# Optimization experiments

Measured on AMD Instinct MI355X. Metric: run time of the kernel, lower is better.

The kernel has to match this reference:

```python
import jax, jax.numpy as jnp
import numpy as np

N = 768          # n_nuclei
EMB = 32         # embedding_dim
RBF = 32         # rbf_dim
CUTOFF = 10.0    # rbf_cutoff
MAXQ = 10        # max(charges)


def _edges(n):
    # fully-connected edge list exactly as in GNN.__call__
    senders = np.arange(n).repeat(n - 1)
    recv = np.arange(n)[None].repeat(n - 1, axis=0)
    recv = (recv + np.arange(n - 1)[:, None] + 1) % n
    return jnp.asarray(senders), jnp.asarray(recv.reshape(-1))


def _mlp2(x, w0, b0, w1, b1=None):
    # AutoMLP(out_dim, depth=2): Dense+silu, Dense (final_bias optional)
    h = jax.nn.silu(x @ w0 + b0)
    y = h @ w1
    return y if b1 is None else y + b1


def _seg_mean(vals, seg, n):
    s = jax.ops.segment_sum(vals, seg, num_segments=n, indices_are_sorted=True)
    c = jax.ops.segment_sum(jnp.ones((vals.shape[0], 1), vals.dtype), seg,
                            num_segments=n, indices_are_sorted=True)
    return s / jnp.maximum(c, 1.0)


def setup_inputs() -> dict:
    key = jax.random.key(0)
    ki = iter(jax.random.split(key, 48))

    def W(din, dout):
        return jax.random.normal(next(ki), (din, dout), jnp.float32) / np.sqrt(din).astype(np.float32)

    def b(d):
        return jax.random.normal(next(ki), (d,), jnp.float32) * 0.01

    return dict(
        nuclei=jax.random.normal(next(ki), (N, 3), jnp.float32) * 3.0,
        charges=jax.random.randint(next(ki), (N,), 0, MAXQ),
        f=(jnp.arange(RBF, dtype=jnp.float32) + 1.0) * jnp.pi,  # BesselRBF param init
        embed_table=jax.random.normal(next(ki), (MAXQ, EMB), jnp.float32),
        mp1_w0=W(96, 32), mp1_b0=b(32), mp1_w1=W(32, 32), mp1_b1=b(32),
        up1_w0=W(64, 64), up1_b0=b(64), up1_w1=W(64, 64), up1_b1=b(64),
        mp2_w0=W(160, 32), mp2_b0=b(32), mp2_w1=W(32, 32), mp2_b1=b(32),
        up2_w0=W(96, 64), up2_b0=b(64), up2_w1=W(64, 64), up2_b1=b(64),
        no_w0=W(160, 3), no_b0=b(3), no_w1=W(3, 3),
        no_embed=jax.random.normal(next(ki), (MAXQ, 3), jnp.float32) * 0.1,
        go_w0=W(160, 1), go_b0=b(1), go_w1=W(1, 1), go_b1=b(1),
    )


def reference(nuclei, charges, f, embed_table,
              mp1_w0, mp1_b0, mp1_w1, mp1_b1,
              up1_w0, up1_b0, up1_w1, up1_b1,
              mp2_w0, mp2_b0, mp2_w1, mp2_b1,
              up2_w0, up2_b0, up2_w1, up2_b1,
              no_w0, no_b0, no_w1, no_embed,
              go_w0, go_b0, go_w1, go_b1):
    nuclei = nuclei.reshape(-1, 3) @ jnp.eye(3, dtype=nuclei.dtype)  # constants 'axes'
    n = nuclei.shape[0]
    senders, receivers = _edges(n)

    # BesselRBF on pairwise distances
    d = jnp.linalg.norm(nuclei[senders] - nuclei[receivers], axis=-1)
    x_ext = d[:, None] + 1e-8
    e_embed = jnp.sqrt(2.0 / CUTOFF) * jnp.sin(f * x_ext / CUTOFF) / x_ext  # [E, RBF]

    n_embed = embed_table[charges]  # [N, EMB]
    embeddings = [n_embed]

    # layer 1: msg out 32, update out 64 (no residual: 32 != 64)
    edge_in = jnp.concatenate([n_embed[senders], n_embed[receivers], e_embed], axis=-1)
    msg = _seg_mean(_mlp2(edge_in, mp1_w0, mp1_b0, mp1_w1, mp1_b1), senders, n)
    upd = _mlp2(jnp.concatenate([n_embed, msg], axis=-1), up1_w0, up1_b0, up1_w1, up1_b1)
    n_embed = upd  # dims differ -> plain replacement
    embeddings.append(n_embed)

    # layer 2: msg out 32, update out 64 (residual: 64 == 64)
    edge_in = jnp.concatenate([n_embed[senders], n_embed[receivers], e_embed], axis=-1)
    msg = _seg_mean(_mlp2(edge_in, mp2_w0, mp2_b0, mp2_w1, mp2_b1), senders, n)
    upd = _mlp2(jnp.concatenate([n_embed, msg], axis=-1), up2_w0, up2_b0, up2_w1, up2_b1)
    n_embed = n_embed + upd
    embeddings.append(n_embed)

    agg = jnp.concatenate(embeddings, axis=-1)  # [N, 32+64+64=160]

    node_out = _mlp2(agg, no_w0, no_b0, no_w1) + no_embed[charges]  # [N, 3]
    global_out = _mlp2(jnp.mean(agg, axis=0), go_w0, go_b0, go_w1, go_b1)  # [1]
    return (node_out, global_out)
```

## Files before the change

### kernel.cpp

```cpp
#include <hip/hip_runtime.h>
#include <hip/hip_bf16.h>

typedef __hip_bfloat16 bf16;
typedef __attribute__((ext_vector_type(8))) short short8;
typedef __attribute__((ext_vector_type(4))) float float4v;

#define NN   768
#define NEPS 767

#define C_NUC   0
#define C_F     2304
#define C_MP1W0 2656
#define C_MP1B0 5728
#define C_MP1W1 5760
#define C_MP1B1 6784
#define C_UP1W0 6816
#define C_UP1B0 10912
#define C_UP1W1 10976
#define C_UP1B1 15072
#define C_MP2W0 15136
#define C_MP2B0 20256
#define C_MP2W1 20288
#define C_MP2B1 21312
#define C_UP2W0 21344
#define C_UP2B0 27488
#define C_UP2W1 27552
#define C_UP2B1 31648
#define C_NOW0  31712
#define C_NOB0  32192
#define C_NOW1  32195
#define C_NOEMB 32204
#define C_GOW0  32234
#define C_GOB0  32394
#define C_GOW1  32395
#define C_GOB1  32396
#define C_ETAB  32400
__device__ __align__(16) float g_c[32720];

#define OFF_EMB1 73728
#define OFF_SA2  122880
#define OFF_SB2  147456
__device__ float g_ws[172032];
__device__ float g_agg[640];
__device__ float g_tab[660];
__device__ int   g_cnt;
__device__ int   g_isf;
__device__ short8 g_rbf[NN*48*64];

struct Ptrs { const void* p[28]; };

__device__ __forceinline__ float b2f(bf16 v){ return __bfloat162float(v); }
__device__ __forceinline__ float LD(const void* p, int i, int f32){
  return f32 ? ((const float*)p)[i] : b2f(((const bf16*)p)[i]);
}
__device__ __forceinline__ int detect_f32(const void* f){
  float v = ((const float*)f)[0];
  return (fabsf(v - 3.14159265f) < 0.01f) ? 1 : 0;
}
__device__ __forceinline__ float fast_rcp(float x){ return __builtin_amdgcn_rcpf(x); }
__device__ __forceinline__ float silu_f(float p){ return p * fast_rcp(1.f + __expf(-p)); }
__device__ __forceinline__ unsigned short rne_bf16(float x){
  unsigned int b = __float_as_uint(x);
  return (unsigned short)((b + 0x7fffu + ((b >> 16) & 1u)) >> 16);
}
__device__ __forceinline__ void cv(const void* p, int off, int sz, int gt, int isf){
  for (int i = gt; i < sz; i += 96*256) g_c[off + i] = LD(p, i, isf);
}

__launch_bounds__(256)
__global__ void k_conv_prep(Ptrs P){
  int t = threadIdx.x;
  int gt = blockIdx.x*256 + t;
  int isf = detect_f32(P.p[2]);
  if (gt == 0){ g_isf = isf; g_cnt = 0; }
  if (gt < 640) g_agg[gt] = 0.f;

  cv(P.p[0],  C_NUC,   2304, gt, isf);
  cv(P.p[2],  C_F,     32,   gt, isf);
  cv(P.p[3],  C_ETAB,  320,  gt, isf);
  cv(P.p[4],  C_MP1W0, 3072, gt, isf);
  cv(P.p[5],  C_MP1B0, 32,   gt, isf);
  cv(P.p[6],  C_MP1W1, 1024, gt, isf);
  cv(P.p[7],  C_MP1B1, 32,   gt, isf);
  cv(P.p[8],  C_UP1W0, 4096, gt, isf);
  cv(P.p[9],  C_UP1B0, 64,   gt, isf);
  cv(P.p[10], C_UP1W1, 4096, gt, isf);
  cv(P.p[11], C_UP1B1, 64,   gt, isf);
  cv(P.p[12], C_MP2W0, 5120, gt, isf);
  cv(P.p[13], C_MP2B0, 32,   gt, isf);
  cv(P.p[14], C_MP2W1, 1024, gt, isf);
  cv(P.p[15], C_MP2B1, 32,   gt, isf);
  cv(P.p[16], C_UP2W0, 6144, gt, isf);
  cv(P.p[17], C_UP2B0, 64,   gt, isf);
  cv(P.p[18], C_UP2W1, 4096, gt, isf);
  cv(P.p[19], C_UP2B1, 64,   gt, isf);
  cv(P.p[20], C_NOW0,  480,  gt, isf);
  cv(P.p[21], C_NOB0,  3,    gt, isf);
  cv(P.p[22], C_NOW1,  9,    gt, isf);
  cv(P.p[23], C_NOEMB, 30,   gt, isf);
  cv(P.p[24], C_GOW0,  160,  gt, isf);
  cv(P.p[25], C_GOB0,  1,    gt, isf);
  cv(P.p[26], C_GOW1,  1,    gt, isf);
  cv(P.p[27], C_GOB1,  1,    gt, isf);

  if (blockIdx.x == 0){
    __shared__ float etabL[320], w0L[2048];
    for (int idx = t; idx < 320;  idx += 256) etabL[idx] = LD(P.p[3], idx, isf);
    for (int idx = t; idx < 2048; idx += 256) w0L[idx]   = LD(P.p[4], idx, isf);
    __syncthreads();
    for (int idx = t; idx < 320; idx += 256){
      int ch = idx >> 5, cc = idx & 31;
      float a = 0.f, b = 0.f;
      #pragma unroll
      for (int k = 0; k < 32; k++){
        float e = etabL[ch*32 + k];
        a = fmaf(e, w0L[k*32 + cc],        a);
        b = fmaf(e, w0L[1024 + k*32 + cc], b);
      }
      g_tab[ch*33 + cc]       = a;
      g_tab[330 + ch*33 + cc] = b;
    }
  }
}

__launch_bounds__(256)
__global__ void k_edge1(const int* __restrict__ charges){
  __shared__ __align__(16) float pos[NN*3];
  __shared__ __align__(16) float w1L[1024];
  __shared__ float TAL[330], TBL[330];
  __shared__ int   chS[NN];
  __shared__ float wsum[4][32];
  __shared__ float hsumL[32];
  __shared__ float msgL[32];
  __shared__ float catU[64], hU[64], e1U[64], part[256];

  int i = blockIdx.x, t = threadIdx.x;
  int w = t >> 6, lane = t & 63, q = lane >> 4, c = lane & 15;

  {
    const float4* src = (const float4*)(g_c + C_NUC);
    float4* dst = (float4*)pos;
    for (int idx = t; idx < 576; idx += 256) dst[idx] = src[idx];
    ((float4*)w1L)[t] = ((const float4*)(g_c + C_MP1W1))[t];
    for (int idx = t; idx < 660; idx += 256){
      float v = g_tab[idx];
      if (idx < 330) TAL[idx] = v; else TBL[idx - 330] = v;
    }
    for (int idx = t; idx < NN; idx += 256) chS[idx] = charges[idx];
  }
  short8 bfr0, bfr1;
  #pragma unroll
  for (int j = 0; j < 8; j++){
    int row = q*8 + j;
    bfr0[j] = (short)rne_bf16(g_c[C_MP1W0 + 2048 + row*32 + c]);
    bfr1[j] = (short)rne_bf16(g_c[C_MP1W0 + 2048 + row*32 + 16 + c]);
  }
  float fj[8];
  #pragma unroll
  for (int j = 0; j < 8; j++) fj[j] = g_c[C_F + q*8 + j] * 0.1f;
  __syncthreads();

  int chI = chS[i];
  float preB0 = TAL[chI*33 + c]      + g_c[C_MP1B0 + c];
  float preB1 = TAL[chI*33 + 16 + c] + g_c[C_MP1B0 + 16 + c];
  float px = pos[i*3], py = pos[i*3+1], pz = pos[i*3+2];

  float xs[12], scv[12];
  #pragma unroll
  for (int s = 0; s < 12; s++){
    int el = (w + s*4)*16 + c;
    int ela = (el < NEPS) ? el : 0;
    int r = ela + (ela >= i);
    float dx = px - pos[r*3], dy = py - pos[r*3+1], dz = pz - pos[r*3+2];
    float d = sqrtf(fmaf(dx, dx, fmaf(dy, dy, dz*dz)));
    xs[s] = d + 1e-8f;
    scv[s] = 0.44721359549995793f * fast_rcp(xs[s]);
  }

  float sum0 = 0.f, sum1 = 0.f;
  #pragma unroll 4
  for (int s = 0; s < 12; s++){
    int tl = w + s*4;
    float sb0[4], sb1[4];
    #pragma unroll
    for (int p = 0; p < 4; p++){
      int el2 = tl*16 + q*4 + p;
      int e2a = (el2 < NEPS) ? el2 : 0;
      int r2 = e2a + (e2a >= i);
      int ch2 = chS[r2];
      sb0[p] = TBL[ch2*33 + c];
      sb1[p] = TBL[ch2*33 + 16 + c];
    }
    short8 af;
    #pragma unroll
    for (int j = 0; j < 8; j++) af[j] = (short)rne_bf16(scv[s] * __sinf(fj[j]*xs[s]));
    g_rbf[(i*48 + tl)*64 + lane] = af;
    float4v z = {0.f, 0.f, 0.f, 0.f};
    float4v a0 = __builtin_amdgcn_mfma_f32_16x16x32_bf16(af, bfr0, z, 0, 0, 0);
    float4v a1 = __builtin_amdgcn_mfma_f32_16x16x32_bf16(af, bfr1, z, 0, 0, 0);
    #pragma unroll
    for (int p = 0; p < 4; p++){
      int el2 = tl*16 + q*4 + p;
      if (el2 < NEPS){
        sum0 += silu_f(a0[p] + preB0 + sb0[p]);
        sum1 += silu_f(a1[p] + preB1 + sb1[p]);
      }
    }
  }
  sum0 += __shfl_xor(sum0, 16); sum0 += __shfl_xor(sum0, 32);
  sum1 += __shfl_xor(sum1, 16); sum1 += __shfl_xor(sum1, 32);
  if (lane < 16){ wsum[w][lane] = sum0; wsum[w][16 + lane] = sum1; }
  __syncthreads();
  if (t < 32) hsumL[t] = wsum[0][t] + wsum[1][t] + wsum[2][t] + wsum[3][t];
  __syncthreads();
  if (t < 32){
    float y = 0.f;
    #pragma unroll
    for (int m = 0; m < 32; m++) y = fmaf(hsumL[m], w1L[m*32 + t], y);
    msgL[t] = y * (1.f/767.f) + g_c[C_MP1B1 + t];
  }

  if (t < 32){
    catU[t] = g_c[C_ETAB + chI*32 + t];
    catU[32 + t] = msgL[t];
  }
  __syncthreads();

  int g = t >> 6, col = t & 63;
  {
    const float* w0 = g_c + C_UP1W0;
    float p0 = 0.f;
    #pragma unroll
    for (int j = 0; j < 16; j++){ int k = g*16 + j; p0 = fmaf(catU[k], w0[k*64 + col], p0); }
    part[t] = p0;
  }
  __syncthreads();
  if (t < 64) hU[t] = silu_f(g_c[C_UP1B0 + t] + part[t] + part[64+t] + part[128+t] + part[192+t]);
  __syncthreads();
  {
    const float* w1u = g_c + C_UP1W1;
    float p1 = 0.f;
    #pragma unroll
    for (int j = 0; j < 16; j++){ int k = g*16 + j; p1 = fmaf(hU[k], w1u[k*64 + col], p1); }
    part[t] = p1;
  }
  __syncthreads();
  if (t < 64){
    float y = g_c[C_UP1B1 + t] + part[t] + part[64+t] + part[128+t] + part[192+t];
    e1U[t] = y;
    g_ws[OFF_EMB1 + i*64 + t] = y;
  }
  __syncthreads();
  {
    int half = t >> 7, g2 = (t >> 5) & 3, c32 = t & 31;
    const float* m2 = g_c + C_MP2W0;
    float p2 = 0.f;
    #pragma unroll
    for (int j = 0; j < 16; j++){
      int k = g2*16 + j;
      p2 = fmaf(e1U[k], m2[(half*64 + k)*32 + c32], p2);
    }
    part[t] = p2;
  }
  __syncthreads();
  if (t < 64){
    int half = t >> 5, c32 = t & 31;
    float s = part[half*128 + c32] + part[half*128 + 32 + c32]
            + part[half*128 + 64 + c32] + part[half*128 + 96 + c32];
    if (half == 0) g_ws[OFF_SA2 + i*32 + c32] = s;
    else           g_ws[OFF_SB2 + i*32 + c32] = s;
  }
}

__launch_bounds__(256)
__global__ void k_edge2(const int* __restrict__ charges, void* __restrict__ out){
  __shared__ __align__(16) float w1L[1024];
  __shared__ float wsum[4][32];
  __shared__ float hsumL[32];
  __shared__ float msgL[32];
  __shared__ float catU[96], hU[64], aggL[160], noL[522], h3L[3], part[256];
  __shared__ int lastL;

  int i = blockIdx.x, t = threadIdx.x;
  int w = t >> 6, lane = t & 63, q = lane >> 4, c = lane & 15;

  ((float4*)w1L)[t] = ((const float4*)(g_c + C_MP2W1))[t];
  const float* SA = g_ws + OFF_SA2;
  const float* SB = g_ws + OFF_SB2;
  short8 bfr0, bfr1;
  #pragma unroll
  for (int j = 0; j < 8; j++){
    int row = q*8 + j;
    bfr0[j] = (short)rne_bf16(g_c[C_MP2W0 + 4096 + row*32 + c]);
    bfr1[j] = (short)rne_bf16(g_c[C_MP2W0 + 4096 + row*32 + 16 + c]);
  }
  float preB0 = SA[i*32 + c]      + g_c[C_MP2B0 + c];
  float preB1 = SA[i*32 + 16 + c] + g_c[C_MP2B0 + 16 + c];

  float sum0 = 0.f, sum1 = 0.f;
  short8 afA = g_rbf[(i*48 + w)*64 + lane];
  float sbA0[4], sbA1[4];
  #pragma unroll
  for (int p = 0; p < 4; p++){
    int el2 = w*16 + q*4 + p;
    int e2a = (el2 < NEPS) ? el2 : 0;
    int r2 = e2a + (e2a >= i);
    sbA0[p] = SB[r2*32 + c];
    sbA1[p] = SB[r2*32 + 16 + c];
  }
  #pragma unroll
  for (int s = 0; s < 12; s++){
    int tl = w + s*4;
    short8 afB;
    float sbB0[4], sbB1[4];
    if (s < 11){
      int tn = tl + 4;
      afB = g_rbf[(i*48 + tn)*64 + lane];
      #pragma unroll
      for (int p = 0; p < 4; p++){
        int el2 = tn*16 + q*4 + p;
        int e2a = (el2 < NEPS) ? el2 : 0;
        int r2 = e2a + (e2a >= i);
        sbB0[p] = SB[r2*32 + c];
        sbB1[p] = SB[r2*32 + 16 + c];
      }
    }
    float4v z = {0.f, 0.f, 0.f, 0.f};
    float4v a0 = __builtin_amdgcn_mfma_f32_16x16x32_bf16(afA, bfr0, z, 0, 0, 0);
    float4v a1 = __builtin_amdgcn_mfma_f32_16x16x32_bf16(afA, bfr1, z, 0, 0, 0);
    #pragma unroll
    for (int p = 0; p < 4; p++){
      int el2 = tl*16 + q*4 + p;
      if (el2 < NEPS){
        sum0 += silu_f(a0[p] + preB0 + sbA0[p]);
        sum1 += silu_f(a1[p] + preB1 + sbA1[p]);
      }
    }
    if (s < 11){
      afA = afB;
      #pragma unroll
      for (int p = 0; p < 4; p++){ sbA0[p] = sbB0[p]; sbA1[p] = sbB1[p]; }
    }
  }
  sum0 += __shfl_xor(sum0, 16); sum0 += __shfl_xor(sum0, 32);
  sum1 += __shfl_xor(sum1, 16); sum1 += __shfl_xor(sum1, 32);
  if (lane < 16){ wsum[w][lane] = sum0; wsum[w][16 + lane] = sum1; }
  __syncthreads();
  if (t < 32) hsumL[t] = wsum[0][t] + wsum[1][t] + wsum[2][t] + wsum[3][t];
  __syncthreads();
  if (t < 32){
    float y = 0.f;
    #pragma unroll
    for (int m = 0; m < 32; m++) y = fmaf(hsumL[m], w1L[m*32 + t], y);
    msgL[t] = y * (1.f/767.f) + g_c[C_MP2B1 + t];
  }

  if (t < 64) catU[t] = g_ws[OFF_EMB1 + i*64 + t];
  if (t < 32){ catU[64 + t] = msgL[t]; aggL[t] = g_c[C_ETAB + charges[i]*32 + t]; }
  for (int idx = t; idx < 522; idx += 256) noL[idx] = g_c[C_NOW0 + idx];
  __syncthreads();

  int g = t >> 6, col = t & 63;
  {
    const float* w0 = g_c + C_UP2W0;
    float p0 = 0.f;
    #pragma unroll
    for (int j = 0; j < 24; j++){ int k = g*24 + j; p0 = fmaf(catU[k], w0[k*64 + col], p0); }
    part[t] = p0;
  }
  __syncthreads();
  if (t < 64) hU[t] = silu_f(g_c[C_UP2B0 + t] + part[t] + part[64+t] + part[128+t] + part[192+t]);
  __syncthreads();
  {
    const float* w1u = g_c + C_UP2W1;
    float p1 = 0.f;
    #pragma unroll
    for (int j = 0; j < 16; j++){ int k = g*16 + j; p1 = fmaf(hU[k], w1u[k*64 + col], p1); }
    part[t] = p1;
  }
  __syncthreads();
  if (t < 64){
    float y = g_c[C_UP2B1 + t] + part[t] + part[64+t] + part[128+t] + part[192+t];
    float e2 = catU[t] + y;
    aggL[32 + t] = catU[t];
    aggL[96 + t] = e2;
  }
  __syncthreads();
  if (t < 48){
    int chunk = t / 3, c3 = t - chunk*3;
    float p = 0.f;
    #pragma unroll
    for (int j = 0; j < 10; j++){ int k = chunk*10 + j; p = fmaf(aggL[k], noL[k*3 + c3], p); }
    part[t] = p;
  }
  __syncthreads();
  if (t < 3){
    float p = noL[480 + t];
    #pragma unroll
    for (int ch = 0; ch < 16; ch++) p += part[ch*3 + t];
    h3L[t] = silu_f(p);
  }
  __syncthreads();
  if (t < 3){
    float o = 0.f;
    #pragma unroll
    for (int m = 0; m < 3; m++) o = fmaf(h3L[m], noL[483 + m*3 + t], o);
    o += noL[492 + charges[i]*3 + t];
    if (g_isf) ((float*)out)[i*3 + t] = o;
    else       ((bf16*)out)[i*3 + t] = __float2bfloat16(o);
  }
  if (t < 160) atomicAdd(&g_agg[(i & 3)*160 + t], aggL[t]);
  __syncthreads();
  if (t == 0) lastL = (atomicAdd(&g_cnt, 1) == NN - 1) ? 1 : 0;
  __syncthreads();
  if (lastL){
    float v = 0.f;
    if (t < 160){
      float s = atomicAdd(&g_agg[t], 0.f) + atomicAdd(&g_agg[160 + t], 0.f)
              + atomicAdd(&g_agg[320 + t], 0.f) + atomicAdd(&g_agg[480 + t], 0.f);
      v = s * (1.f/768.f) * g_c[C_GOW0 + t];
    }
    part[t] = v;
    __syncthreads();
    if (t == 0){
      float tot = 0.f;
      for (int k = 0; k < 160; k++) tot += part[k];
      float h = silu_f(tot + g_c[C_GOB0]);
      float go = h * g_c[C_GOW1] + g_c[C_GOB1];
      if (g_isf) ((float*)out)[2304] = go;
      else       ((bf16*)out)[2304] = __float2bfloat16(go);
    }
  }
}

extern "C" void kernel_launch(void* const* d_in, const int* in_sizes, int n_in,
                              void* d_out, int out_size, void* d_ws, size_t ws_size,
                              hipStream_t stream) {
  Ptrs P;
  for (int k = 0; k < 28; k++) P.p[k] = d_in[k];
  const int* charges = (const int*)d_in[1];

  k_conv_prep<<<96, 256, 0, stream>>>(P);
  k_edge1<<<NN, 256, 0, stream>>>(charges);
  k_edge2<<<NN, 256, 0, stream>>>(charges, d_out);
}
```

Measured before the change: 165.0 us.

## Drop prep kernel and rbf buffer; recompute RBF in edge2, read inputs directly

Removes the separate conversion/prep kernel. Each edge kernel now reads weights directly from the input pointers, converting fp32 or bf16 on the fly, and computes the charge-embedding projections per block. The stored bf16 RBF buffer (about 4.7 MB written by edge1 and read back by edge2) is gone; edge2 recomputes distances and sin-based RBFs itself. The goal is to save one launch and the global-memory round trip, at the cost of redundant per-block weight loads and precomputation, extra transcendental work in edge2, and loss of the explicit prefetch pipelining.

Result: slower. 173.8 us (+5.4%).

```diff
diff --git a/kernel.cpp b/kernel.cpp
--- a/kernel.cpp
+++ b/kernel.cpp
@@ -8,44 +8,11 @@
 #define NN   768
 #define NEPS 767
 
-#define C_NUC   0
-#define C_F     2304
-#define C_MP1W0 2656
-#define C_MP1B0 5728
-#define C_MP1W1 5760
-#define C_MP1B1 6784
-#define C_UP1W0 6816
-#define C_UP1B0 10912
-#define C_UP1W1 10976
-#define C_UP1B1 15072
-#define C_MP2W0 15136
-#define C_MP2B0 20256
-#define C_MP2W1 20288
-#define C_MP2B1 21312
-#define C_UP2W0 21344
-#define C_UP2B0 27488
-#define C_UP2W1 27552
-#define C_UP2B1 31648
-#define C_NOW0  31712
-#define C_NOB0  32192
-#define C_NOW1  32195
-#define C_NOEMB 32204
-#define C_GOW0  32234
-#define C_GOB0  32394
-#define C_GOW1  32395
-#define C_GOB1  32396
-#define C_ETAB  32400
-__device__ __align__(16) float g_c[32720];
-
-#define OFF_EMB1 73728
-#define OFF_SA2  122880
-#define OFF_SB2  147456
-__device__ float g_ws[172032];
+__device__ float g_emb1[NN*64];
+__device__ float g_sa2[NN*32];
+__device__ float g_sb2[NN*32];
 __device__ float g_agg[640];
-__device__ float g_tab[660];
 __device__ int   g_cnt;
-__device__ int   g_isf;
-__device__ short8 g_rbf[NN*48*64];
 
 struct Ptrs { const void* p[28]; };
 
@@ -63,108 +30,89 @@
   unsigned int b = __float_as_uint(x);
   return (unsigned short)((b + 0x7fffu + ((b >> 16) & 1u)) >> 16);
 }
-__device__ __forceinline__ void cv(const void* p, int off, int sz, int gt, int isf){
-  for (int i = gt; i < sz; i += 96*256) g_c[off + i] = LD(p, i, isf);
+
+template<int NJ>
+__device__ __forceinline__ float dotn(const void* wp, int base, int stride, int col,
+                                      const float* x, int k0, int isf){
+  float p = 0.f;
+  if (isf){
+    const float* f = (const float*)wp;
+    #pragma unroll
+    for (int j = 0; j < NJ; j++){ int k = k0 + j; p = fmaf(x[k], f[base + k*stride + col], p); }
+  } else {
+    const bf16* h = (const bf16*)wp;
+    #pragma unroll
+    for (int j = 0; j < NJ; j++){ int k = k0 + j; p = fmaf(x[k], b2f(h[base + k*stride + col]), p); }
+  }
+  return p;
 }
 
 __launch_bounds__(256)
-__global__ void k_conv_prep(Ptrs P){
-  int t = threadIdx.x;
-  int gt = blockIdx.x*256 + t;
-  int isf = detect_f32(P.p[2]);
-  if (gt == 0){ g_isf = isf; g_cnt = 0; }
-  if (gt < 640) g_agg[gt] = 0.f;
-
-  cv(P.p[0],  C_NUC,   2304, gt, isf);
-  cv(P.p[2],  C_F,     32,   gt, isf);
-  cv(P.p[3],  C_ETAB,  320,  gt, isf);
-  cv(P.p[4],  C_MP1W0, 3072, gt, isf);
-  cv(P.p[5],  C_MP1B0, 32,   gt, isf);
-  cv(P.p[6],  C_MP1W1, 1024, gt, isf);
-  cv(P.p[7],  C_MP1B1, 32,   gt, isf);
-  cv(P.p[8],  C_UP1W0, 4096, gt, isf);
-  cv(P.p[9],  C_UP1B0, 64,   gt, isf);
-  cv(P.p[10], C_UP1W1, 4096, gt, isf);
-  cv(P.p[11], C_UP1B1, 64,   gt, isf);
-  cv(P.p[12], C_MP2W0, 5120, gt, isf);
-  cv(P.p[13], C_MP2B0, 32,   gt, isf);
-  cv(P.p[14], C_MP2W1, 1024, gt, isf);
-  cv(P.p[15], C_MP2B1, 32,   gt, isf);
-  cv(P.p[16], C_UP2W0, 6144, gt, isf);
-  cv(P.p[17], C_UP2B0, 64,   gt, isf);
-  cv(P.p[18], C_UP2W1, 4096, gt, isf);
-  cv(P.p[19], C_UP2B1, 64,   gt, isf);
-  cv(P.p[20], C_NOW0,  480,  gt, isf);
-  cv(P.p[21], C_NOB0,  3,    gt, isf);
-  cv(P.p[22], C_NOW1,  9,    gt, isf);
-  cv(P.p[23], C_NOEMB, 30,   gt, isf);
-  cv(P.p[24], C_GOW0,  160,  gt, isf);
-  cv(P.p[25], C_GOB0,  1,    gt, isf);
-  cv(P.p[26], C_GOW1,  1,    gt, isf);
-  cv(P.p[27], C_GOB1,  1,    gt, isf);
-
-  if (blockIdx.x == 0){
-    __shared__ float etabL[320], w0L[2048];
-    for (int idx = t; idx < 320;  idx += 256) etabL[idx] = LD(P.p[3], idx, isf);
-    for (int idx = t; idx < 2048; idx += 256) w0L[idx]   = LD(P.p[4], idx, isf);
-    __syncthreads();
-    for (int idx = t; idx < 320; idx += 256){
-      int ch = idx >> 5, cc = idx & 31;
-      float a = 0.f, b = 0.f;
-      #pragma unroll
-      for (int k = 0; k < 32; k++){
-        float e = etabL[ch*32 + k];
-        a = fmaf(e, w0L[k*32 + cc],        a);
-        b = fmaf(e, w0L[1024 + k*32 + cc], b);
-      }
-      g_tab[ch*33 + cc]       = a;
-      g_tab[330 + ch*33 + cc] = b;
-    }
-  }
-}
-
-__launch_bounds__(256)
-__global__ void k_edge1(const int* __restrict__ charges){
+__global__ void k_edge1(Ptrs P, const int* __restrict__ charges){
   __shared__ __align__(16) float pos[NN*3];
-  __shared__ __align__(16) float w1L[1024];
-  __shared__ float TAL[330], TBL[330];
+  __shared__ float etabL[320];
+  __shared__ __align__(16) float w0F[2048];
+  __shared__ float TBL[330];
   __shared__ int   chS[NN];
-  __shared__ float wsum[4][32];
-  __shared__ float hsumL[32];
-  __shared__ float msgL[32];
+  __shared__ float w1L[1024];
+  __shared__ float wsum[4][32], hsumL[32], msgL[32];
   __shared__ float catU[64], hU[64], e1U[64], part[256];
 
   int i = blockIdx.x, t = threadIdx.x;
   int w = t >> 6, lane = t & 63, q = lane >> 4, c = lane & 15;
-
-  {
-    const float4* src = (const float4*)(g_c + C_NUC);
-    float4* dst = (float4*)pos;
-    for (int idx = t; idx < 576; idx += 256) dst[idx] = src[idx];
-    ((float4*)w1L)[t] = ((const float4*)(g_c + C_MP1W1))[t];
-    for (int idx = t; idx < 660; idx += 256){
-      float v = g_tab[idx];
-      if (idx < 330) TAL[idx] = v; else TBL[idx - 330] = v;
-    }
-    for (int idx = t; idx < NN; idx += 256) chS[idx] = charges[idx];
-  }
+  int isf = detect_f32(P.p[2]);
+
+  if (i == 0){
+    for (int idx = t; idx < 640; idx += 256) g_agg[idx] = 0.f;
+    if (t == 0) g_cnt = 0;
+  }
+  for (int idx = t; idx < NN*3; idx += 256) pos[idx]   = LD(P.p[0], idx, isf);
+  for (int idx = t; idx < 320;  idx += 256) etabL[idx] = LD(P.p[3], idx, isf);
+  for (int idx = t; idx < 2048; idx += 256) w0F[idx]   = LD(P.p[4], idx, isf);
+  for (int idx = t; idx < 1024; idx += 256) w1L[idx]   = LD(P.p[6], idx, isf);
+  for (int idx = t; idx < NN;   idx += 256) chS[idx]   = charges[idx];
+
   short8 bfr0, bfr1;
-  #pragma unroll
-  for (int j = 0; j < 8; j++){
-    int row = q*8 + j;
-    bfr0[j] = (short)rne_bf16(g_c[C_MP1W0 + 2048 + row*32 + c]);
-    bfr1[j] = (short)rne_bf16(g_c[C_MP1W0 + 2048 + row*32 + 16 + c]);
+  if (isf){
+    const float* wp = (const float*)P.p[4];
+    #pragma unroll
+    for (int j = 0; j < 8; j++){
+      int row = q*8 + j;
+      bfr0[j] = (short)rne_bf16(wp[2048 + row*32 + c]);
+      bfr1[j] = (short)rne_bf16(wp[2048 + row*32 + 16 + c]);
+    }
+  } else {
+    const short* wp = (const short*)P.p[4];
+    #pragma unroll
+    for (int j = 0; j < 8; j++){
+      int row = q*8 + j;
+      bfr0[j] = wp[2048 + row*32 + c];
+      bfr1[j] = wp[2048 + row*32 + 16 + c];
+    }
   }
   float fj[8];
   #pragma unroll
-  for (int j = 0; j < 8; j++) fj[j] = g_c[C_F + q*8 + j] * 0.1f;
-  __syncthreads();
-
+  for (int j = 0; j < 8; j++) fj[j] = LD(P.p[2], q*8 + j, isf) * 0.1f;
+  __syncthreads();
+
+  for (int idx = t; idx < 320; idx += 256){
+    int ch = idx >> 5, cc = idx & 31;
+    float b = 0.f;
+    #pragma unroll
+    for (int k = 0; k < 32; k++) b = fmaf(etabL[ch*32 + k], w0F[1024 + k*32 + cc], b);
+    TBL[ch*33 + cc] = b;
+  }
   int chI = chS[i];
-  float preB0 = TAL[chI*33 + c]      + g_c[C_MP1B0 + c];
-  float preB1 = TAL[chI*33 + 16 + c] + g_c[C_MP1B0 + 16 + c];
+  float preB0 = LD(P.p[5], c, isf), preB1 = LD(P.p[5], 16 + c, isf);
+  #pragma unroll
+  for (int k = 0; k < 32; k++){
+    float e = etabL[chI*32 + k];
+    preB0 = fmaf(e, w0F[k*32 + c],      preB0);
+    preB1 = fmaf(e, w0F[k*32 + 16 + c], preB1);
+  }
+  __syncthreads();
+
   float px = pos[i*3], py = pos[i*3+1], pz = pos[i*3+2];
-
   float xs[12], scv[12];
   #pragma unroll
   for (int s = 0; s < 12; s++){
@@ -194,7 +142,6 @@
     short8 af;
     #pragma unroll
     for (int j = 0; j < 8; j++) af[j] = (short)rne_bf16(scv[s] * __sinf(fj[j]*xs[s]));
-    g_rbf[(i*48 + tl)*64 + lane] = af;
     float4v z = {0.f, 0.f, 0.f, 0.f};
     float4v a0 = __builtin_amdgcn_mfma_f32_16x16x32_bf16(af, bfr0, z, 0, 0, 0);
     float4v a1 = __builtin_amdgcn_mfma_f32_16x16x32_bf16(af, bfr1, z, 0, 0, 0);
@@ -217,129 +164,125 @@
     float y = 0.f;
     #pragma unroll
     for (int m = 0; m < 32; m++) y = fmaf(hsumL[m], w1L[m*32 + t], y);
-    msgL[t] = y * (1.f/767.f) + g_c[C_MP1B1 + t];
-  }
-
-  if (t < 32){
-    catU[t] = g_c[C_ETAB + chI*32 + t];
-    catU[32 + t] = msgL[t];
-  }
+    msgL[t] = y * (1.f/767.f) + LD(P.p[7], t, isf);
+  }
+  if (t < 32){ catU[t] = etabL[chI*32 + t]; catU[32 + t] = msgL[t]; }
   __syncthreads();
 
   int g = t >> 6, col = t & 63;
-  {
-    const float* w0 = g_c + C_UP1W0;
-    float p0 = 0.f;
-    #pragma unroll
-    for (int j = 0; j < 16; j++){ int k = g*16 + j; p0 = fmaf(catU[k], w0[k*64 + col], p0); }
-    part[t] = p0;
-  }
-  __syncthreads();
-  if (t < 64) hU[t] = silu_f(g_c[C_UP1B0 + t] + part[t] + part[64+t] + part[128+t] + part[192+t]);
-  __syncthreads();
-  {
-    const float* w1u = g_c + C_UP1W1;
-    float p1 = 0.f;
-    #pragma unroll
-    for (int j = 0; j < 16; j++){ int k = g*16 + j; p1 = fmaf(hU[k], w1u[k*64 + col], p1); }
-    part[t] = p1;
-  }
+  part[t] = dotn<16>(P.p[8], 0, 64, col, catU, g*16, isf);
+  __syncthreads();
+  if (t < 64) hU[t] = silu_f(LD(P.p[9], t, isf) + part[t] + part[64+t] + part[128+t] + part[192+t]);
+  __syncthreads();
+  part[t] = dotn<16>(P.p[10], 0, 64, col, hU, g*16, isf);
   __syncthreads();
   if (t < 64){
-    float y = g_c[C_UP1B1 + t] + part[t] + part[64+t] + part[128+t] + part[192+t];
+    float y = LD(P.p[11], t, isf) + part[t] + part[64+t] + part[128+t] + part[192+t];
     e1U[t] = y;
-    g_ws[OFF_EMB1 + i*64 + t] = y;
+    g_emb1[i*64 + t] = y;
   }
   __syncthreads();
   {
     int half = t >> 7, g2 = (t >> 5) & 3, c32 = t & 31;
-    const float* m2 = g_c + C_MP2W0;
-    float p2 = 0.f;
-    #pragma unroll
-    for (int j = 0; j < 16; j++){
-      int k = g2*16 + j;
-      p2 = fmaf(e1U[k], m2[(half*64 + k)*32 + c32], p2);
-    }
-    part[t] = p2;
+    part[t] = dotn<16>(P.p[12], half*2048, 32, c32, e1U, g2*16, isf);
   }
   __syncthreads();
   if (t < 64){
-    int half = t >> 5, c32 = t & 31;
-    float s = part[half*128 + c32] + part[half*128 + 32 + c32]
-            + part[half*128 + 64 + c32] + part[half*128 + 96 + c32];
-    if (half == 0) g_ws[OFF_SA2 + i*32 + c32] = s;
-    else           g_ws[OFF_SB2 + i*32 + c32] = s;
+    int half2 = t >> 5, cc = t & 31;
+    float s = part[half2*128 + cc] + part[half2*128 + 32 + cc]
+            + part[half2*128 + 64 + cc] + part[half2*128 + 96 + cc];
+    if (half2 == 0) g_sa2[i*32 + cc] = s;
+    else            g_sb2[i*32 + cc] = s;
   }
 }
 
 __launch_bounds__(256)
-__global__ void k_edge2(const int* __restrict__ charges, void* __restrict__ out){
-  __shared__ __align__(16) float w1L[1024];
-  __shared__ float wsum[4][32];
-  __shared__ float hsumL[32];
-  __shared__ float msgL[32];
-  __shared__ float catU[96], hU[64], aggL[160], noL[522], h3L[3], part[256];
+__global__ void k_edge2(Ptrs P, const int* __restrict__ charges, void* __restrict__ out){
+  __shared__ __align__(16) float pos[NN*3];
+  __shared__ float w1L[1024];
+  __shared__ float noL[522];
+  __shared__ float wsum[4][32], hsumL[32], msgL[32];
+  __shared__ float catU[96], hU[64], aggL[160], h3L[3], part[256];
   __shared__ int lastL;
 
   int i = blockIdx.x, t = threadIdx.x;
   int w = t >> 6, lane = t & 63, q = lane >> 4, c = lane & 15;
-
-  ((float4*)w1L)[t] = ((const float4*)(g_c + C_MP2W1))[t];
-  const float* SA = g_ws + OFF_SA2;
-  const float* SB = g_ws + OFF_SB2;
-  short8 bfr0, bfr1;
-  #pragma unroll
-  for (int j = 0; j < 8; j++){
-    int row = q*8 + j;
-    bfr0[j] = (short)rne_bf16(g_c[C_MP2W0 + 4096 + row*32 + c]);
-    bfr1[j] = (short)rne_bf16(g_c[C_MP2W0 + 4096 + row*32 + 16 + c]);
-  }
-  float preB0 = SA[i*32 + c]      + g_c[C_MP2B0 + c];
-  float preB1 = SA[i*32 + 16 + c] + g_c[C_MP2B0 + 16 + c];
+  int isf = detect_f32(P.p[2]);
+
+  for (int idx = t; idx < NN*3; idx += 256) pos[idx] = LD(P.p[0], idx, isf);
+  for (int idx = t; idx < 1024; idx += 256) w1L[idx] = LD(P.p[14], idx, isf);
+  for (int idx = t; idx < 522; idx += 256){
+    float v;
+    if      (idx < 480) v = LD(P.p[20], idx, isf);
+    else if (idx < 483) v = LD(P.p[21], idx - 480, isf);
+    else if (idx < 492) v = LD(P.p[22], idx - 483, isf);
+    else                v = LD(P.p[23], idx - 492, isf);
+    noL[idx] = v;
+  }
+  short8 cfr0, cfr1;
+  if (isf){
+    const float* wp = (const float*)P.p[12];
+    #pragma unroll
+    for (int j = 0; j < 8; j++){
+      int row = q*8 + j;
+      cfr0[j] = (short)rne_bf16(wp[4096 + row*32 + c]);
+      cfr1[j] = (short)rne_bf16(wp[4096 + row*32 + 16 + c]);
+    }
+  } else {
+    const short* wp = (const short*)P.p[12];
+    #pragma unroll
+    for (int j = 0; j < 8; j++){
+      int row = q*8 + j;
+      cfr0[j] = wp[4096 + row*32 + c];
+      cfr1[j] = wp[4096 + row*32 + 16 + c];
+    }
+  }
+  float fj[8];
+  #pragma unroll
+  for (int j = 0; j < 8; j++) fj[j] = LD(P.p[2], q*8 + j, isf) * 0.1f;
+  float preC0 = g_sa2[i*32 + c]      + LD(P.p[13], c, isf);
+  float preC1 = g_sa2[i*32 + 16 + c] + LD(P.p[13], 16 + c, isf);
+  __syncthreads();
+
+  float px = pos[i*3], py = pos[i*3+1], pz = pos[i*3+2];
+  float xs[12], scv[12];
+  #pragma unroll
+  for (int s = 0; s < 12; s++){
+    int el = (w + s*4)*16 + c;
+    int ela = (el < NEPS) ? el : 0;
+    int r = ela + (ela >= i);
+    float dx = px - pos[r*3], dy = py - pos[r*3+1], dz = pz - pos[r*3+2];
+    float d = sqrtf(fmaf(dx, dx, fmaf(dy, dy, dz*dz)));
+    xs[s] = d + 1e-8f;
+    scv[s] = 0.44721359549995793f * fast_rcp(xs[s]);
+  }
 
   float sum0 = 0.f, sum1 = 0.f;
-  short8 afA = g_rbf[(i*48 + w)*64 + lane];
-  float sbA0[4], sbA1[4];
-  #pragma unroll
-  for (int p = 0; p < 4; p++){
-    int el2 = w*16 + q*4 + p;
-    int e2a = (el2 < NEPS) ? el2 : 0;
-    int r2 = e2a + (e2a >= i);
-    sbA0[p] = SB[r2*32 + c];
-    sbA1[p] = SB[r2*32 + 16 + c];
-  }
-  #pragma unroll
+  #pragma unroll 4
   for (int s = 0; s < 12; s++){
     int tl = w + s*4;
-    short8 afB;
-    float sbB0[4], sbB1[4];
-    if (s < 11){
-      int tn = tl + 4;
-      afB = g_rbf[(i*48 + tn)*64 + lane];
-      #pragma unroll
-      for (int p = 0; p < 4; p++){
-        int el2 = tn*16 + q*4 + p;
-        int e2a = (el2 < NEPS) ? el2 : 0;
-        int r2 = e2a + (e2a >= i);
-        sbB0[p] = SB[r2*32 + c];
-        sbB1[p] = SB[r2*32 + 16 + c];
-      }
-    }
+    float sb0[4], sb1[4];
+    #pragma unroll
+    for (int p = 0; p < 4; p++){
+      int el2 = tl*16 + q*4 + p;
+      int e2a = (el2 < NEPS) ? el2 : 0;
+      int r2 = e2a + (e2a >= i);
+      sb0[p] = g_sb2[r2*32 + c];
+      sb1[p] = g_sb2[r2*32 + 16 + c];
+    }
+    short8 af;
+    #pragma unroll
+    for (int j = 0; j < 8; j++) af[j] = (short)rne_bf16(scv[s] * __sinf(fj[j]*xs[s]));
     float4v z = {0.f, 0.f, 0.f, 0.f};
-    float4v a0 = __builtin_amdgcn_mfma_f32_16x16x32_bf16(afA, bfr0, z, 0, 0, 0);
-    float4v a1 = __builtin_amdgcn_mfma_f32_16x16x32_bf16(afA, bfr1, z, 0, 0, 0);
+    float4v a0 = __builtin_amdgcn_mfma_f32_16x16x32_bf16(af, cfr0, z, 0, 0, 0);
+    float4v a1 = __builtin_amdgcn_mfma_f32_16x16x32_bf16(af, cfr1, z, 0, 0, 0);
     #pragma unroll
     for (int p = 0; p < 4; p++){
       int el2 = tl*16 + q*4 + p;
       if (el2 < NEPS){
-        sum0 += silu_f(a0[p] + preB0 + sbA0[p]);
-        sum1 += silu_f(a1[p] + preB1 + sbA1[p]);
+        sum0 += silu_f(a0[p] + preC0 + sb0[p]);
+        sum1 += silu_f(a1[p] + preC1 + sb1[p]);
       }
-    }
-    if (s < 11){
-      afA = afB;
-      #pragma unroll
-      for (int p = 0; p < 4; p++){ sbA0[p] = sbB0[p]; sbA1[p] = sbB1[p]; }
     }
   }
   sum0 += __shfl_xor(sum0, 16); sum0 += __shfl_xor(sum0, 32);
@@ -352,35 +295,22 @@
     float y = 0.f;
     #pragma unroll
     for (int m = 0; m < 32; m++) y = fmaf(hsumL[m], w1L[m*32 + t], y);
-    msgL[t] = y * (1.f/767.f) + g_c[C_MP2B1 + t];
-  }
-
-  if (t < 64) catU[t] = g_ws[OFF_EMB1 + i*64 + t];
-  if (t < 32){ catU[64 + t] = msgL[t]; aggL[t] = g_c[C_ETAB + charges[i]*32 + t]; }
-  for (int idx = t; idx < 522; idx += 256) noL[idx] = g_c[C_NOW0 + idx];
+    msgL[t] = y * (1.f/767.f) + LD(P.p[15], t, isf);
+  }
+  int chI = charges[i];
+  if (t < 64) catU[t] = g_emb1[i*64 + t];
+  if (t < 32){ catU[64 + t] = msgL[t]; aggL[t] = LD(P.p[3], chI*32 + t, isf); }
   __syncthreads();
 
   int g = t >> 6, col = t & 63;
-  {
-    const float* w0 = g_c + C_UP2W0;
-    float p0 = 0.f;
-    #pragma unroll
-    for (int j = 0; j < 24; j++){ int k = g*24 + j; p0 = fmaf(catU[k], w0[k*64 + col], p0); }
-    part[t] = p0;
-  }
-  __syncthreads();
-  if (t < 64) hU[t] = silu_f(g_c[C_UP2B0 + t] + part[t] + part[64+t] + part[128+t] + part[192+t]);
-  __syncthreads();
-  {
-    const float* w1u = g_c + C_UP2W1;
-    float p1 = 0.f;
-    #pragma unroll
-    for (int j = 0; j < 16; j++){ int k = g*16 + j; p1 = fmaf(hU[k], w1u[k*64 + col], p1); }
-    part[t] = p1;
-  }
+  part[t] = dotn<24>(P.p[16], 0, 64, col, catU, g*24, isf);
+  __syncthreads();
+  if (t < 64) hU[t] = silu_f(LD(P.p[17], t, isf) + part[t] + part[64+t] + part[128+t] + part[192+t]);
+  __syncthreads();
+  part[t] = dotn<16>(P.p[18], 0, 64, col, hU, g*16, isf);
   __syncthreads();
   if (t < 64){
-    float y = g_c[C_UP2B1 + t] + part[t] + part[64+t] + part[128+t] + part[192+t];
+    float y = LD(P.p[19], t, isf) + part[t] + part[64+t] + part[128+t] + part[192+t];
     float e2 = catU[t] + y;
     aggL[32 + t] = catU[t];
     aggL[96 + t] = e2;
@@ -405,9 +335,9 @@
     float o = 0.f;
     #pragma unroll
     for (int m = 0; m < 3; m++) o = fmaf(h3L[m], noL[483 + m*3 + t], o);
-    o += noL[492 + charges[i]*3 + t];
-    if (g_isf) ((float*)out)[i*3 + t] = o;
-    else       ((bf16*)out)[i*3 + t] = __float2bfloat16(o);
+    o += noL[492 + chI*3 + t];
+    if (isf) ((float*)out)[i*3 + t] = o;
+    else     ((bf16*)out)[i*3 + t] = __float2bfloat16(o);
   }
   if (t < 160) atomicAdd(&g_agg[(i & 3)*160 + t], aggL[t]);
   __syncthreads();
@@ -418,17 +348,17 @@
     if (t < 160){
       float s = atomicAdd(&g_agg[t], 0.f) + atomicAdd(&g_agg[160 + t], 0.f)
               + atomicAdd(&g_agg[320 + t], 0.f) + atomicAdd(&g_agg[480 + t], 0.f);
-      v = s * (1.f/768.f) * g_c[C_GOW0 + t];
+      v = s * (1.f/768.f) * LD(P.p[24], t, isf);
     }
     part[t] = v;
     __syncthreads();
     if (t == 0){
       float tot = 0.f;
       for (int k = 0; k < 160; k++) tot += part[k];
-      float h = silu_f(tot + g_c[C_GOB0]);
-      float go = h * g_c[C_GOW1] + g_c[C_GOB1];
-      if (g_isf) ((float*)out)[2304] = go;
-      else       ((bf16*)out)[2304] = __float2bfloat16(go);
+      float h = silu_f(tot + LD(P.p[25], 0, isf));
+      float go = h * LD(P.p[26], 0, isf) + LD(P.p[27], 0, isf);
+      if (isf) ((float*)out)[2304] = go;
+      else     ((bf16*)out)[2304] = __float2bfloat16(go);
     }
   }
 }
@@ -440,7 +370,6 @@
   for (int k = 0; k < 28; k++) P.p[k] = d_in[k];
   const int* charges = (const int*)d_in[1];
 
-  k_conv_prep<<<96, 256, 0, stream>>>(P);
-  k_edge1<<<NN, 256, 0, stream>>>(charges);
-  k_edge2<<<NN, 256, 0, stream>>>(charges, d_out);
-}
+  k_edge1<<<NN, 256, 0, stream>>>(P, charges);
+  k_edge2<<<NN, 256, 0, stream>>>(P, charges, d_out);
+}
```
